# Kernel optimization log

Hardware: AMD Instinct MI355X
Metric: run time of the kernel (lower is better)

## Reference

```python
import jax, jax.numpy as jnp
import numpy as np
import math

B, N, D, H, HC = 2, 2048, 1024, 16, 8
HIDDEN = 4 * D
MAX_PERIOD = 10000.0


def _timestep_embedding(t, dim):
    half = dim // 2
    freqs = jnp.exp(-math.log(MAX_PERIOD) * jnp.arange(half, dtype=jnp.float32) / half)
    args = t[:, None] * freqs[None, :]
    return jnp.concatenate([jnp.cos(args), jnp.sin(args)], axis=-1)


def _layer_norm(x, scale, bias, eps=1e-6):
    mu = jnp.mean(x, axis=-1, keepdims=True)
    var = jnp.mean(jnp.square(x - mu), axis=-1, keepdims=True)
    return (x - mu) * jax.lax.rsqrt(var + eps) * scale + bias


def _modulate(x, shift, scale):
    return x * (1.0 + scale[:, None, :]) + shift[:, None, :]


def setup_inputs():
    key = jax.random.key(0)
    ks = jax.random.split(key, 16)

    def dense(k, fin, fout):
        return jax.random.normal(k, (fin, fout), dtype=jnp.float32) / np.sqrt(fin)

    return {
        'x': jax.random.normal(ks[0], (B, N, D), dtype=jnp.float32),
        't': jax.random.uniform(ks[1], (B,), dtype=jnp.float32) * 1000.0,
        'norm1_scale': jnp.ones((D,), jnp.float32),
        'norm1_bias': jnp.zeros((D,), jnp.float32),
        'norm2_scale': jnp.ones((D,), jnp.float32),
        'norm2_bias': jnp.zeros((D,), jnp.float32),
        'tc_w1': dense(ks[2], HIDDEN, HIDDEN),
        'tc_b1': jnp.zeros((HIDDEN,), jnp.float32),
        'tc_w2': dense(ks[3], HIDDEN, HIDDEN),
        'tc_b2': jnp.zeros((HIDDEN,), jnp.float32),
        'tc_wa': 0.02 * dense(ks[4], HIDDEN, 4 * D),
        'tc_ba': jnp.zeros((4 * D,), jnp.float32),
        'tc_wc': 0.02 * dense(ks[5], HIDDEN, 4 * D),
        'tc_bc': jnp.zeros((4 * D,), jnp.float32),
        'attn_qk_w': dense(ks[6], D, D),
        'attn_v_w': dense(ks[7], D, D),
        'attn_out_w': dense(ks[8], D, D),
        'doob_w': 0.02 * dense(ks[9], D, 1),
        'doob_b': jnp.zeros((1,), jnp.float32),
        'ch_qk_w': dense(ks[10], D, D),
        'ch_v_w': dense(ks[11], D, D),
        'ch_out_w': dense(ks[12], D, D),
        'tau': jnp.ones((HC, 1, 1), jnp.float32),
        'gamma1': 1e-4 * jnp.ones((D,), jnp.float32),
        'gamma2': 1e-4 * jnp.ones((D,), jnp.float32),
    }


def reference(x, t, norm1_scale, norm1_bias, norm2_scale, norm2_bias,
              tc_w1, tc_b1, tc_w2, tc_b2, tc_wa, tc_ba, tc_wc, tc_bc,
              attn_qk_w, attn_v_w, attn_out_w, doob_w, doob_b,
              ch_qk_w, ch_v_w, ch_out_w, tau, gamma1, gamma2):
    # ---- AdaLN time conditioning ----
    emb = _timestep_embedding(t, HIDDEN)                 # (B, HIDDEN)
    h = jax.nn.silu(emb @ tc_w1 + tc_b1)
    h = jax.nn.silu(h @ tc_w2 + tc_b2)
    a_shift, a_scale, a_gate, a_lg = jnp.split(h @ tc_wa + tc_ba, 4, axis=-1)
    c_shift, c_scale, c_gate, c_lg = jnp.split(h @ tc_wc + tc_bc, 4, axis=-1)

    # ---- token-diffusion attention (MHDM, tied Q=K, Doob tilt) ----
    x1 = _modulate(_layer_norm(x, norm1_scale, norm1_bias), a_shift, a_scale)
    qk = (x1 @ attn_qk_w) * jnp.exp(a_lg)[:, None, :]    # (B,N,D)
    v = x1 @ attn_v_w
    dh = D // H
    qh = qk.reshape(B, N, H, dh).transpose(0, 2, 1, 3)   # (B,H,N,dh)
    vh = v.reshape(B, N, H, dh).transpose(0, 2, 1, 3)
    dot = jnp.einsum('bhmd,bhnd->bhmn', qh, qh)
    q2 = jnp.sum(qh * qh, axis=-1)
    logits = 2.0 * dot - q2[:, :, :, None] - q2[:, :, None, :]
    phi = (x1 @ doob_w + doob_b)[..., 0]                 # (B,N) destination tilt
    logits = logits + phi[:, None, None, :]
    attn = jax.nn.softmax(logits, axis=-1)
    w = jnp.einsum('bhmn,bhnd->bhmd', attn, vh)
    attn_out = w.transpose(0, 2, 1, 3).reshape(B, N, D) @ attn_out_w
    x = x + attn_out * a_gate[:, None, :] * gamma1

    # ---- channel-diffusion attention ----
    x2 = _modulate(_layer_norm(x, norm2_scale, norm2_bias), c_shift, c_scale)
    qkc = (x2 @ ch_qk_w) * jnp.exp(c_lg)[:, None, :]
    vc = x2 @ ch_v_w
    dhc = D // HC
    qkc = qkc.transpose(0, 2, 1).reshape(B, HC, dhc, N)  # (B,HC,dhc,N)
    vc = vc.transpose(0, 2, 1).reshape(B, HC, dhc, N)
    dotc = jnp.einsum('bhcn,bhdn->bhcd', qkc, qkc)
    q2c = jnp.sum(qkc * qkc, axis=-1)                    # (B,HC,dhc)
    logitsc = (2.0 * dotc - q2c[:, :, :, None] - q2c[:, :, None, :]) / math.sqrt(N)
    logitsc = logitsc * tau[None, ...]
    attnc = jax.nn.softmax(logitsc, axis=-1)
    wc = jnp.einsum('bhcd,bhdn->bhcn', attnc, vc)
    ch_out = wc.reshape(B, D, N).transpose(0, 2, 1) @ ch_out_w
    x = x + ch_out * c_gate[:, None, :] * gamma2
    return x
```

## Files before the change

### kernel.cpp

```cpp
#include <hip/hip_runtime.h>
#include <hip/hip_bf16.h>
#include <math.h>

typedef __bf16 bf16;
typedef bf16 bf16x8 __attribute__((ext_vector_type(8)));
typedef bf16 bf16x2 __attribute__((ext_vector_type(2)));
typedef float f32x4 __attribute__((ext_vector_type(4)));

#define B_   2
#define N_   2048
#define D_   1024
#define H_   16
#define HC_  8
#define M_   (B_*N_)

__device__ __forceinline__ void gl16(const bf16* g, bf16* lds_base) {
#if __has_builtin(__builtin_amdgcn_global_load_lds)
  __builtin_amdgcn_global_load_lds((const __attribute__((address_space(1))) void*)g,
                                   (__attribute__((address_space(3))) void*)lds_base,
                                   16, 0, 0);
#else
  int lane = threadIdx.x & 63;
  *(uint4*)(lds_base + lane * 8) = *(const uint4*)g;
#endif
}

__device__ __forceinline__ bf16x2 cvt_pk_bf16(float lo, float hi) {
  unsigned int r;
  asm("v_cvt_pk_bf16_f32 %0, %1, %2" : "=v"(r) : "v"(lo), "v"(hi));
  union { unsigned int u; bf16x2 v; } c;
  c.u = r;
  return c.v;
}

__global__ __launch_bounds__(256) void emb_kernel(const float* __restrict__ tin,
                                                  float* __restrict__ emb) {
  int idx = blockIdx.x * 256 + threadIdx.x;
  int b = idx >> 12, p = idx & 4095;
  float tv = tin[b];
  int half = p & 2047;
  float freq = expf(-logf(10000.f) * (float)half * (1.f / 2048.f));
  float arg = tv * freq;
  emb[idx] = (p < 2048) ? cosf(arg) : sinf(arg);
}

__global__ __launch_bounds__(256) void gemv_kernel(const float* __restrict__ x,
                                                   const float* __restrict__ W,
                                                   float* __restrict__ part) {
  __shared__ float xs[2][64];
  int t = threadIdx.x;
  int j0 = blockIdx.x * 512;
  int k0 = blockIdx.y * 64;
  if (t < 64) xs[0][t] = x[k0 + t];
  else if (t < 128) xs[1][t - 64] = x[4096 + k0 + (t - 64)];
  __syncthreads();
  float a00 = 0.f, a01 = 0.f, a10 = 0.f, a11 = 0.f;
  int j = j0 + t * 2;
  #pragma unroll 8
  for (int k = 0; k < 64; k++) {
    float2 wv = *(const float2*)(W + (size_t)(k0 + k) * 4096 + j);
    float x0 = xs[0][k], x1 = xs[1][k];
    a00 += x0 * wv.x; a01 += x0 * wv.y;
    a10 += x1 * wv.x; a11 += x1 * wv.y;
  }
  *(float2*)(part + (size_t)(blockIdx.y * 2 + 0) * 4096 + j) = make_float2(a00, a01);
  *(float2*)(part + (size_t)(blockIdx.y * 2 + 1) * 4096 + j) = make_float2(a10, a11);
}

__global__ __launch_bounds__(256) void gemv_reduce_kernel(const float* __restrict__ part,
                                                          const float* __restrict__ bias,
                                                          float* __restrict__ y, int act) {
  int idx = blockIdx.x * 256 + threadIdx.x;
  int b = idx >> 12, j = idx & 4095;
  float s = bias[j];
  #pragma unroll
  for (int kc = 0; kc < 64; kc++) s += part[(size_t)(kc * 2 + b) * 4096 + j];
  if (act) s = s / (1.f + expf(-s));
  y[idx] = s;
}

__global__ __launch_bounds__(256) void postA_kernel(const float* __restrict__ avec,
                                                    const float* __restrict__ cvec,
                                                    const float* __restrict__ g1,
                                                    const float* __restrict__ g2,
                                                    float* __restrict__ sca, float* __restrict__ scc,
                                                    float* __restrict__ agv, float* __restrict__ cgv) {
  int idx = blockIdx.x * 256 + threadIdx.x;
  int b = idx >> 10, d = idx & 1023;
  sca[idx] = expf(avec[b * 4096 + 3072 + d]);
  scc[idx] = expf(cvec[b * 4096 + 3072 + d]);
  agv[idx] = avec[b * 4096 + 2048 + d] * g1[d];
  cgv[idx] = cvec[b * 4096 + 2048 + d] * g2[d];
}

__global__ __launch_bounds__(256) void wtconv6_kernel(const float* w0, const float* w1,
                                                      const float* w2, const float* w3,
                                                      const float* w4, const float* w5,
                                                      bf16* o0, bf16* o1, bf16* o2,
                                                      bf16* o3, bf16* o4, bf16* o5) {
  const float* W; bf16* Wt;
  switch (blockIdx.z) {
    case 0: W = w0; Wt = o0; break;
    case 1: W = w1; Wt = o1; break;
    case 2: W = w2; Wt = o2; break;
    case 3: W = w3; Wt = o3; break;
    case 4: W = w4; Wt = o4; break;
    default: W = w5; Wt = o5; break;
  }
  __shared__ float tile[32][33];
  int t = threadIdx.x;
  int i = t >> 5, j = t & 31;
  int n0 = blockIdx.x * 32, k0 = blockIdx.y * 32;
  #pragma unroll
  for (int u = 0; u < 4; u++) {
    int k = i + u * 8;
    tile[k][j] = W[(size_t)(k0 + k) * 1024 + n0 + j];
  }
  __syncthreads();
  #pragma unroll
  for (int u = 0; u < 4; u++) {
    int n = i + u * 8;
    Wt[(size_t)(n0 + n) * 1024 + k0 + j] = (bf16)tile[j][n];
  }
}

__global__ __launch_bounds__(256) void ln_mod_kernel(const float* __restrict__ xin,
                                                     const float* __restrict__ nsc,
                                                     const float* __restrict__ nbi,
                                                     const float* __restrict__ mod,
                                                     const float* __restrict__ doobw,
                                                     float* __restrict__ phi,
                                                     bf16* __restrict__ outp) {
  int row = blockIdx.x;
  int b = row >> 11;
  int t = threadIdx.x;
  const float* xr = xin + (size_t)row * 1024;
  float v[4], s = 0.f, ss = 0.f;
  #pragma unroll
  for (int u = 0; u < 4; u++) { v[u] = xr[t + u * 256]; s += v[u]; ss += v[u] * v[u]; }
  #pragma unroll
  for (int off = 1; off < 64; off <<= 1) { s += __shfl_xor(s, off, 64); ss += __shfl_xor(ss, off, 64); }
  __shared__ float sb[4], ssb[4], pb[4];
  if ((t & 63) == 0) { sb[t >> 6] = s; ssb[t >> 6] = ss; }
  __syncthreads();
  s = sb[0] + sb[1] + sb[2] + sb[3];
  ss = ssb[0] + ssb[1] + ssb[2] + ssb[3];
  float mu = s * (1.f / 1024.f);
  float var = ss * (1.f / 1024.f) - mu * mu;
  float rs = rsqrtf(var + 1e-6f);
  const float* shv = mod + b * 4096;
  const float* scv = mod + b * 4096 + 1024;
  float ph = 0.f;
  #pragma unroll
  for (int u = 0; u < 4; u++) {
    int d = t + u * 256;
    float y = (v[u] - mu) * rs * nsc[d] + nbi[d];
    float ym = y * (1.f + scv[d]) + shv[d];
    outp[(size_t)row * 1024 + d] = (bf16)ym;
    if (doobw) ph += ym * doobw[d];
  }
  if (doobw) {
    #pragma unroll
    for (int off = 1; off < 64; off <<= 1) ph += __shfl_xor(ph, off, 64);
    if ((t & 63) == 0) pb[t >> 6] = ph;
    __syncthreads();
    if (t == 0) phi[row] = pb[0] + pb[1] + pb[2] + pb[3];
  }
}

__global__ __launch_bounds__(256) void phimax_kernel(const float* __restrict__ phi,
                                                     float* __restrict__ pm) {
  int b = blockIdx.x;
  int t = threadIdx.x;
  float m = -1e30f;
  #pragma unroll
  for (int u = 0; u < 8; u++) m = fmaxf(m, phi[b * 2048 + t + u * 256]);
  #pragma unroll
  for (int off = 1; off < 64; off <<= 1) m = fmaxf(m, __shfl_xor(m, off, 64));
  __shared__ float mb[4];
  if ((t & 63) == 0) mb[t >> 6] = m;
  __syncthreads();
  if (t == 0) pm[b] = fmaxf(fmaxf(mb[0], mb[1]), fmaxf(mb[2], mb[3]));
}

template <int MODE, int TM>
__global__ __launch_bounds__(256) void gemm_kernel(const bf16* __restrict__ A,
                                                   const bf16* __restrict__ Wt,
                                                   const float* __restrict__ scale,
                                                   const float* __restrict__ resid,
                                                   void* __restrict__ out0,
                                                   void* __restrict__ out1) {
  constexpr int K = 1024;
  constexpr int WM = TM / 2;
  constexpr int IT = WM / 16;
  __shared__ bf16 As[TM * 64];
  __shared__ bf16 Bs[128 * 64];
  const int m0 = blockIdx.x * TM;
  const int n0 = blockIdx.y * 128;
  const int t = threadIdx.x, lane = t & 63, wid = t >> 6;
  const int wy = wid >> 1, wx = wid & 1;
  const int ml = lane & 15, quad = lane >> 4, rq = quad * 4, kq = quad * 8;
  const int srow = lane >> 3;
  const int schunk = (lane & 7) ^ srow;
  const bf16* gA = A  + (size_t)(m0 + wid * (TM / 4) + srow) * K + schunk * 8;
  const bf16* gB = Wt + (size_t)(n0 + wid * 32 + srow) * K + schunk * 8;
  bf16* lA = As + (wid * (TM / 4)) * 64;
  bf16* lB = Bs + (wid * 32) * 64;
  const int mlm = ml & 7;

  f32x4 acc[IT][4] = {};
  for (int k0 = 0; k0 < K; k0 += 64) {
    __syncthreads();
    #pragma unroll
    for (int q = 0; q < TM / 32; q++)
      gl16(gA + (size_t)q * 8 * K + k0, lA + q * 8 * 64);
    #pragma unroll
    for (int q = 0; q < 4; q++)
      gl16(gB + (size_t)q * 8 * K + k0, lB + q * 8 * 64);
    __syncthreads();
    #pragma unroll
    for (int ks = 0; ks < 2; ks++) {
      const int slot = ((ks * 4 + quad) ^ mlm) * 8;
      bf16x8 af[IT], bfv[4];
      #pragma unroll
      for (int i = 0; i < IT; i++)
        af[i] = *(const bf16x8*)(As + (wy * WM + i * 16 + ml) * 64 + slot);
      #pragma unroll
      for (int j = 0; j < 4; j++)
        bfv[j] = *(const bf16x8*)(Bs + (wx * 64 + j * 16 + ml) * 64 + slot);
      #pragma unroll
      for (int i = 0; i < IT; i++)
        #pragma unroll
        for (int j = 0; j < 4; j++)
          acc[i][j] = __builtin_amdgcn_mfma_f32_16x16x32_bf16(af[i], bfv[j], acc[i][j], 0, 0, 0);
    }
  }
  #pragma unroll
  for (int i = 0; i < IT; i++) {
    #pragma unroll
    for (int j = 0; j < 4; j++) {
      int col = n0 + wx * 64 + j * 16 + ml;
      #pragma unroll
      for (int r = 0; r < 4; r++) {
        int row = m0 + wy * WM + i * 16 + rq + r;
        int b = row >> 11, n = row & 2047;
        float val = acc[i][j][r];
        if constexpr (MODE == 10) {
          if (col < 1024) {
            ((bf16*)out0)[(size_t)row * 1024 + col] = (bf16)(val * scale[b * 1024 + col]);
          } else {
            int c2 = col - 1024;
            ((bf16*)out1)[((size_t)((b * 16 + (c2 >> 6)) * 64 + (c2 & 63))) * 2048 + n] = (bf16)val;
          }
        } else if constexpr (MODE == 11) {
          if (col < 1024) {
            float sv = val * scale[b * 1024 + col];
            ((bf16*)out0)[((size_t)((b * 8 + (col >> 7)) * 128 + (col & 127))) * 2048 + n] = (bf16)sv;
          } else {
            ((bf16*)out1)[(size_t)row * 1024 + (col - 1024)] = (bf16)val;
          }
        } else {
          float g = scale[b * 1024 + col];
          ((float*)out0)[(size_t)row * 1024 + col] =
              resid[(size_t)row * 1024 + col] + val * g;
        }
      }
    }
  }
}

__global__ __launch_bounds__(256) void q2e_kernel(const bf16* __restrict__ qk,
                                                  const float* __restrict__ phi,
                                                  const float* __restrict__ pm,
                                                  float* __restrict__ q2buf,
                                                  float* __restrict__ ebuf) {
  int row = blockIdx.x;
  int b = row >> 11, n = row & 2047;
  int t = threadIdx.x;
  const bf16* qr = qk + (size_t)row * 1024;
  __shared__ float q2s[16][17];
  {
    int h = t >> 4, i0 = (t & 15) * 4;
    float q = 0.f;
    #pragma unroll
    for (int u = 0; u < 4; u++) { float qv = (float)qr[h * 64 + i0 + u]; q += qv * qv; }
    q2s[h][t & 15] = q;
  }
  __syncthreads();
  if (t < 16) {
    float q2 = 0.f;
    #pragma unroll
    for (int u = 0; u < 16; u++) q2 += q2s[t][u];
    q2buf[(size_t)(b * 16 + t) * 2048 + n] = q2 * 1.44269504f;
    ebuf [(size_t)(b * 16 + t) * 2048 + n] = (phi[row] - q2 - pm[b]) * 1.44269504f;
  }
}

__global__ __launch_bounds__(512, 4) void flash_kernel(const bf16* __restrict__ qk,
                                                       const bf16* __restrict__ vt,
                                                       const float* __restrict__ q2buf,
                                                       const float* __restrict__ ebuf,
                                                       bf16* __restrict__ wout) {
  int mt = blockIdx.x, bh = blockIdx.y;
  int b = bh >> 4, h = bh & 15;
  int m0 = mt * 128;
  int t = threadIdx.x, lane = t & 63, w = t >> 6;
  int ml = lane & 15, quad = lane >> 4;
  int mlm = ml & 7, q1 = quad & 1, qh = quad >> 1;

  __shared__ __align__(16) bf16 Ks[2][64 * 64];
  __shared__ __align__(16) bf16 Vs[2][64 * 64];
  __shared__ __align__(16) bf16 Ps[8 * 16 * 64];

  int sr = lane >> 3, swz = (lane & 7) ^ sr;
  const bf16* gK = qk + (size_t)(b * 2048 + 8 * w + sr) * 1024 + h * 64 + swz * 8;
  const bf16* gV = vt + (size_t)(bh * 64 + 8 * w + sr) * 2048 + swz * 8;

  const bf16* qrow = qk + (size_t)(b * 2048 + m0 + w * 16 + ml) * 1024 + h * 64;
  bf16x8 qf0 = *(const bf16x8*)(qrow + quad * 8);
  bf16x8 qf1 = *(const bf16x8*)(qrow + 32 + quad * 8);

  float q2l = q2buf[(size_t)bh * 2048 + m0 + w * 16 + ml];
  const float* ep = ebuf + (size_t)bh * 2048;

  bf16* Pb = Ps + (w * 16 + ml) * 64;
  f32x4 oacc[4] = {};
  float rs = 0.f;

  gl16(gK, &Ks[0][w * 512]);
  gl16(gV, &Vs[0][w * 512]);

  #pragma unroll 2
  for (int nc = 0; nc < 32; nc++) {
    int cur = nc & 1;
    __syncthreads();
    if (nc + 1 < 32) {
      gl16(gK + (size_t)(nc + 1) * 64 * 1024, &Ks[cur ^ 1][w * 512]);
      gl16(gV + (nc + 1) * 64,                &Vs[cur ^ 1][w * 512]);
    }
    const bf16* Kc = Ks[cur];
    const bf16* Vc = Vs[cur];

    f32x4 sacc[4] = {};
    __builtin_amdgcn_s_setprio(1);
    #pragma unroll
    for (int ks = 0; ks < 2; ks++) {
      bf16x8 qb = ks ? qf1 : qf0;
      #pragma unroll
      for (int j = 0; j < 4; j++) {
        bf16x8 ka = *(const bf16x8*)(Kc + (j * 16 + ml) * 64 + ((4 * ks + quad) ^ mlm) * 8);
        sacc[j] = __builtin_amdgcn_mfma_f32_16x16x32_bf16(ka, qb, sacc[j], 0, 0, 0);
      }
    }
    __builtin_amdgcn_s_setprio(0);

    const float* epc = ep + nc * 64;
    #pragma unroll
    for (int j = 0; j < 4; j++) {
      float4 ev = *(const float4*)(epc + j * 16 + quad * 4);
      float p0 = exp2f(fmaf(2.88539008f, sacc[j][0], ev.x - q2l));
      float p1 = exp2f(fmaf(2.88539008f, sacc[j][1], ev.y - q2l));
      float p2 = exp2f(fmaf(2.88539008f, sacc[j][2], ev.z - q2l));
      float p3 = exp2f(fmaf(2.88539008f, sacc[j][3], ev.w - q2l));
      rs += (p0 + p1) + (p2 + p3);
      int sl = (((2 * j + qh) ^ mlm) * 4 + 2 * q1) * 2;
      *(bf16x2*)(Pb + sl)     = cvt_pk_bf16(p0, p1);
      *(bf16x2*)(Pb + sl + 2) = cvt_pk_bf16(p2, p3);
    }
    __builtin_amdgcn_sched_barrier(0);

    __builtin_amdgcn_s_setprio(1);
    #pragma unroll
    for (int ks = 0; ks < 2; ks++) {
      bf16x8 pa = *(const bf16x8*)(Pb + ((4 * ks + quad) ^ mlm) * 8);
      #pragma unroll
      for (int jd = 0; jd < 4; jd++) {
        bf16x8 vb = *(const bf16x8*)(Vc + (jd * 16 + ml) * 64 + ((4 * ks + quad) ^ mlm) * 8);
        oacc[jd] = __builtin_amdgcn_mfma_f32_16x16x32_bf16(pa, vb, oacc[jd], 0, 0, 0);
      }
    }
    __builtin_amdgcn_s_setprio(0);
  }

  rs += __shfl_xor(rs, 16, 64);
  rs += __shfl_xor(rs, 32, 64);
  float rinv = 1.f / rs;

  int rq = quad * 4;
  float rv[4];
  #pragma unroll
  for (int r = 0; r < 4; r++) rv[r] = __shfl(rinv, rq + r, 64);

  bf16* wrow = wout + (size_t)(b * 2048 + m0 + w * 16) * 1024 + h * 64;
  #pragma unroll
  for (int jd = 0; jd < 4; jd++)
    #pragma unroll
    for (int r = 0; r < 4; r++)
      wrow[(size_t)(rq + r) * 1024 + jd * 16 + ml] = (bf16)(oacc[jd][r] * rv[r]);
}

__global__ __launch_bounds__(256) void gram_kernel(const bf16* __restrict__ qkct,
                                                   float* __restrict__ dotp) {
  int bh = blockIdx.x, ksl = blockIdx.y;
  const bf16* Q = qkct + (size_t)bh * 128 * 2048 + ksl * 256;
  __shared__ bf16 Ts[128 * 40];
  int t = threadIdx.x, lane = t & 63, w = t >> 6;
  int ml = lane & 15, kq = (lane >> 4) * 8, rq = (lane >> 4) * 4;
  f32x4 acc[2][8] = {};
  for (int k0 = 0; k0 < 256; k0 += 32) {
    __syncthreads();
    #pragma unroll
    for (int u = 0; u < 2; u++) {
      int idx = u * 256 + t;
      int r = idx >> 2, seg = (idx & 3) * 8;
      *(uint4*)(Ts + r * 40 + seg) = *(const uint4*)(Q + (size_t)r * 2048 + k0 + seg);
    }
    __syncthreads();
    bf16x8 afr[2], bfr[8];
    #pragma unroll
    for (int i = 0; i < 2; i++) afr[i] = *(const bf16x8*)(Ts + (w * 32 + i * 16 + ml) * 40 + kq);
    #pragma unroll
    for (int j = 0; j < 8; j++) bfr[j] = *(const bf16x8*)(Ts + (j * 16 + ml) * 40 + kq);
    #pragma unroll
    for (int i = 0; i < 2; i++)
      #pragma unroll
      for (int j = 0; j < 8; j++)
        acc[i][j] = __builtin_amdgcn_mfma_f32_16x16x32_bf16(afr[i], bfr[j], acc[i][j], 0, 0, 0);
  }
  float* outp = dotp + ((size_t)ksl * 16 + bh) * 16384;
  #pragma unroll
  for (int i = 0; i < 2; i++)
    #pragma unroll
    for (int j = 0; j < 8; j++)
      #pragma unroll
      for (int r = 0; r < 4; r++) {
        int c = w * 32 + i * 16 + rq + r, d = j * 16 + ml;
        outp[c * 128 + d] = acc[i][j][r];
      }
}

__global__ __launch_bounds__(128) void chsm_kernel(const float* __restrict__ dotp,
                                                   const float* __restrict__ tau,
                                                   bf16* __restrict__ attnc) {
  int blk = blockIdx.x;
  int bh = blk >> 7, c = blk & 127, hc = bh & 7;
  int d = threadIdx.x;
  float dot = 0.f, dd = 0.f;
  #pragma unroll
  for (int kc = 0; kc < 8; kc++) {
    const float* pp = dotp + ((size_t)kc * 16 + bh) * 16384;
    dot += pp[c * 128 + d];
    dd  += pp[d * 128 + d];
  }
  __shared__ float diag[128];
  __shared__ float red[2], red2[2];
  diag[d] = dd;
  __syncthreads();
  float qc = diag[c];
  float sc = tau[hc] * rsqrtf(2048.f);
  float lg = sc * (2.f * dot - qc - dd);
  float mx = lg;
  #pragma unroll
  for (int off = 1; off < 64; off <<= 1) mx = fmaxf(mx, __shfl_xor(mx, off, 64));
  if ((d & 63) == 0) red[d >> 6] = mx;
  __syncthreads();
  mx = fmaxf(red[0], red[1]);
  float e = exp2f((lg - mx) * 1.44269504f);
  float sm = e;
  #pragma unroll
  for (int off = 1; off < 64; off <<= 1) sm += __shfl_xor(sm, off, 64);
  if ((d & 63) == 0) red2[d >> 6] = sm;
  __syncthreads();
  sm = red2[0] + red2[1];
  attnc[(size_t)bh * 16384 + c * 128 + d] = (bf16)(e / sm);
}

__global__ __launch_bounds__(256) void chav_kernel(const bf16* __restrict__ attnc,
                                                   const bf16* __restrict__ vc,
                                                   bf16* __restrict__ wcn) {
  int nb = blockIdx.x, bh = blockIdx.y;
  int b = bh >> 3, hc = bh & 7;
  int n0 = nb * 64;
  __shared__ bf16 As[128 * 136];
  __shared__ bf16 Bs[64 * 136];
  int t = threadIdx.x, lane = t & 63, w = t >> 6;
  int ml = lane & 15, kq = (lane >> 4) * 8, rq = (lane >> 4) * 4;
  #pragma unroll
  for (int u = 0; u < 8; u++) {
    int idx = u * 256 + t;
    int r = idx >> 4, seg = (idx & 15) * 8;
    *(uint4*)(As + r * 136 + seg) = *(const uint4*)(attnc + (size_t)bh * 16384 + r * 128 + seg);
  }
  #pragma unroll
  for (int u = 0; u < 4; u++) {
    int idx = u * 256 + t;
    int r = idx >> 4, seg = (idx & 15) * 8;
    *(uint4*)(Bs + r * 136 + seg) =
        *(const uint4*)(vc + (size_t)(b * 2048 + n0 + r) * 1024 + hc * 128 + seg);
  }
  __syncthreads();
  f32x4 acc[2][4] = {};
  #pragma unroll
  for (int ks = 0; ks < 4; ks++) {
    bf16x8 afr[2], bfr[4];
    #pragma unroll
    for (int i = 0; i < 2; i++)
      afr[i] = *(const bf16x8*)(As + (w * 32 + i * 16 + ml) * 136 + ks * 32 + kq);
    #pragma unroll
    for (int j = 0; j < 4; j++)
      bfr[j] = *(const bf16x8*)(Bs + (j * 16 + ml) * 136 + ks * 32 + kq);
    #pragma unroll
    for (int i = 0; i < 2; i++)
      #pragma unroll
      for (int j = 0; j < 4; j++)
        acc[i][j] = __builtin_amdgcn_mfma_f32_16x16x32_bf16(afr[i], bfr[j], acc[i][j], 0, 0, 0);
  }
  #pragma unroll
  for (int i = 0; i < 2; i++)
    #pragma unroll
    for (int j = 0; j < 4; j++)
      #pragma unroll
      for (int r = 0; r < 4; r++) {
        int c = w * 32 + i * 16 + rq + r;
        int n = n0 + j * 16 + ml;
        wcn[(size_t)(b * 2048 + n) * 1024 + hc * 128 + c] = (bf16)acc[i][j][r];
      }
}

extern "C" void kernel_launch(void* const* d_in, const int* in_sizes, int n_in,
                              void* d_out, int out_size, void* d_ws, size_t ws_size,
                              hipStream_t stream) {
  const float* x      = (const float*)d_in[0];
  const float* t      = (const float*)d_in[1];
  const float* n1s    = (const float*)d_in[2];
  const float* n1b    = (const float*)d_in[3];
  const float* n2s    = (const float*)d_in[4];
  const float* n2b    = (const float*)d_in[5];
  const float* tc_w1  = (const float*)d_in[6];
  const float* tc_b1  = (const float*)d_in[7];
  const float* tc_w2  = (const float*)d_in[8];
  const float* tc_b2  = (const float*)d_in[9];
  const float* tc_wa  = (const float*)d_in[10];
  const float* tc_ba  = (const float*)d_in[11];
  const float* tc_wc  = (const float*)d_in[12];
  const float* tc_bc  = (const float*)d_in[13];
  const float* aqk_w  = (const float*)d_in[14];
  const float* av_w   = (const float*)d_in[15];
  const float* aout_w = (const float*)d_in[16];
  const float* doobw  = (const float*)d_in[17];
  const float* cqk_w  = (const float*)d_in[19];
  const float* cv_w   = (const float*)d_in[20];
  const float* cout_w = (const float*)d_in[21];
  const float* tau    = (const float*)d_in[22];
  const float* g1     = (const float*)d_in[23];
  const float* g2     = (const float*)d_in[24];
  float* out = (float*)d_out;

  char* p = (char*)d_ws;
  auto alloc = [&](size_t bytes) -> void* {
    void* r = (void*)p;
    p += (bytes + 255) & ~(size_t)255;
    return r;
  };
  float* emb   = (float*)alloc(2 * 4096 * 4);
  float* h1    = (float*)alloc(2 * 4096 * 4);
  float* h2    = (float*)alloc(2 * 4096 * 4);
  float* avec  = (float*)alloc(2 * 4096 * 4);
  float* cvec  = (float*)alloc(2 * 4096 * 4);
  float* sca   = (float*)alloc(2 * 1024 * 4);
  float* scc   = (float*)alloc(2 * 1024 * 4);
  float* agv   = (float*)alloc(2 * 1024 * 4);
  float* cgv   = (float*)alloc(2 * 1024 * 4);
  float* phi   = (float*)alloc(4096 * 4);
  float* pmax  = (float*)alloc(2 * 4);
  float* q2buf = (float*)alloc(2 * 16 * 2048 * 4);
  float* ebuf  = (float*)alloc(2 * 16 * 2048 * 4);
  float* dotp  = (float*)alloc((size_t)8 * 16 * 16384 * 4);
  bf16* attnc  = (bf16*)alloc(16 * 128 * 128 * 2);
  bf16* wt     = (bf16*)alloc((size_t)6 * 1024 * 1024 * 2);
  bf16* xbf    = (bf16*)alloc((size_t)M_ * 1024 * 2);
  bf16* qkbf   = (bf16*)alloc((size_t)M_ * 1024 * 2);
  bf16* vbuf   = (bf16*)alloc((size_t)M_ * 1024 * 2);
  bf16* wbuf   = (bf16*)alloc((size_t)M_ * 1024 * 2);
  (void)ws_size; (void)in_sizes; (void)n_in; (void)out_size;

  float* partA = dotp;
  float* partB = dotp + (size_t)64 * 2 * 4096;

  bf16* wt_tok  = wt;
  bf16* wt_out  = wt + (size_t)2 * 1048576;
  bf16* wt_ch   = wt + (size_t)3 * 1048576;
  bf16* wt_cout = wt + (size_t)5 * 1048576;

  dim3 blk(256);
  wtconv6_kernel<<<dim3(32, 32, 6), blk, 0, stream>>>(
      aqk_w, av_w, aout_w, cqk_w, cv_w, cout_w,
      wt_tok, wt_tok + (size_t)1048576, wt_out,
      wt_ch,  wt_ch  + (size_t)1048576, wt_cout);

  emb_kernel<<<32, blk, 0, stream>>>(t, emb);
  gemv_kernel<<<dim3(8, 64), blk, 0, stream>>>(emb, tc_w1, partA);
  gemv_reduce_kernel<<<32, blk, 0, stream>>>(partA, tc_b1, h1, 1);
  gemv_kernel<<<dim3(8, 64), blk, 0, stream>>>(h1, tc_w2, partA);
  gemv_reduce_kernel<<<32, blk, 0, stream>>>(partA, tc_b2, h2, 1);
  gemv_kernel<<<dim3(8, 64), blk, 0, stream>>>(h2, tc_wa, partA);
  gemv_kernel<<<dim3(8, 64), blk, 0, stream>>>(h2, tc_wc, partB);
  gemv_reduce_kernel<<<32, blk, 0, stream>>>(partA, tc_ba, avec, 0);
  gemv_reduce_kernel<<<32, blk, 0, stream>>>(partB, tc_bc, cvec, 0);
  postA_kernel<<<8, blk, 0, stream>>>(avec, cvec, g1, g2, sca, scc, agv, cgv);

  ln_mod_kernel<<<4096, blk, 0, stream>>>(x, n1s, n1b, avec, doobw, phi, xbf);
  phimax_kernel<<<2, blk, 0, stream>>>(phi, pmax);
  gemm_kernel<10, 128><<<dim3(32, 16), blk, 0, stream>>>(xbf, wt_tok, sca, nullptr, qkbf, vbuf);
  q2e_kernel<<<4096, blk, 0, stream>>>(qkbf, phi, pmax, q2buf, ebuf);
  flash_kernel<<<dim3(16, 32), dim3(512), 0, stream>>>(qkbf, vbuf, q2buf, ebuf, wbuf);
  gemm_kernel<4, 64><<<dim3(64, 8), blk, 0, stream>>>(wbuf, wt_out, agv, x, out, nullptr);

  ln_mod_kernel<<<4096, blk, 0, stream>>>(out, n2s, n2b, cvec, nullptr, nullptr, xbf);
  gemm_kernel<11, 128><<<dim3(32, 16), blk, 0, stream>>>(xbf, wt_ch, scc, nullptr, qkbf, vbuf);
  gram_kernel<<<dim3(16, 8), blk, 0, stream>>>(qkbf, dotp);
  chsm_kernel<<<2048, dim3(128), 0, stream>>>(dotp, tau, attnc);
  chav_kernel<<<dim3(32, 16), blk, 0, stream>>>(attnc, vbuf, wbuf);
  gemm_kernel<4, 64><<<dim3(64, 8), blk, 0, stream>>>(wbuf, wt_cout, cgv, out, out, nullptr);
}
```

Measured before the change: 643.1 us.

## Store QK/V head-major and tiled for contiguous flash loads; halve GEMV split-K

The token QK projection is now written head-major as (b,h,n,64), and V is written in 64x64 tiles, so each flash-attention K/V chunk becomes one contiguous 8KB block instead of a strided gather. q2e is rewritten to read a contiguous 64-element row per thread and launches 16x fewer blocks. The timestep-MLP GEMVs use a K-split of 128 rather than 64, which halves the partial buffers and the reduction work. Those partial buffers get their own workspace allocation instead of aliasing dotp. The tradeoff is more scattered stores from the GEMM epilogue.

```diff
diff --git a/kernel.cpp b/kernel.cpp
--- a/kernel.cpp
+++ b/kernel.cpp
@@ -47,17 +47,17 @@
 __global__ __launch_bounds__(256) void gemv_kernel(const float* __restrict__ x,
                                                    const float* __restrict__ W,
                                                    float* __restrict__ part) {
-  __shared__ float xs[2][64];
+  __shared__ float xs[2][128];
   int t = threadIdx.x;
   int j0 = blockIdx.x * 512;
-  int k0 = blockIdx.y * 64;
-  if (t < 64) xs[0][t] = x[k0 + t];
-  else if (t < 128) xs[1][t - 64] = x[4096 + k0 + (t - 64)];
+  int k0 = blockIdx.y * 128;
+  if (t < 128) xs[0][t] = x[k0 + t];
+  else         xs[1][t - 128] = x[4096 + k0 + (t - 128)];
   __syncthreads();
   float a00 = 0.f, a01 = 0.f, a10 = 0.f, a11 = 0.f;
   int j = j0 + t * 2;
   #pragma unroll 8
-  for (int k = 0; k < 64; k++) {
+  for (int k = 0; k < 128; k++) {
     float2 wv = *(const float2*)(W + (size_t)(k0 + k) * 4096 + j);
     float x0 = xs[0][k], x1 = xs[1][k];
     a00 += x0 * wv.x; a01 += x0 * wv.y;
@@ -74,7 +74,7 @@
   int b = idx >> 12, j = idx & 4095;
   float s = bias[j];
   #pragma unroll
-  for (int kc = 0; kc < 64; kc++) s += part[(size_t)(kc * 2 + b) * 4096 + j];
+  for (int kc = 0; kc < 32; kc++) s += part[(size_t)(kc * 2 + b) * 4096 + j];
   if (act) s = s / (1.f + expf(-s));
   y[idx] = s;
 }
@@ -247,10 +247,14 @@
         float val = acc[i][j][r];
         if constexpr (MODE == 10) {
           if (col < 1024) {
-            ((bf16*)out0)[(size_t)row * 1024 + col] = (bf16)(val * scale[b * 1024 + col]);
+            int h = col >> 6, dh = col & 63;
+            ((bf16*)out0)[((size_t)(b * 16 + h) * 2048 + n) * 64 + dh] =
+                (bf16)(val * scale[b * 1024 + col]);
           } else {
             int c2 = col - 1024;
-            ((bf16*)out1)[((size_t)((b * 16 + (c2 >> 6)) * 64 + (c2 & 63))) * 2048 + n] = (bf16)val;
+            int h = c2 >> 6, dh = c2 & 63;
+            ((bf16*)out1)[(((size_t)(b * 16 + h) * 32 + (n >> 6)) * 64 + dh) * 64 + (n & 63)] =
+                (bf16)val;
           }
         } else if constexpr (MODE == 11) {
           if (col < 1024) {
@@ -269,35 +273,28 @@
   }
 }
 
-__global__ __launch_bounds__(256) void q2e_kernel(const bf16* __restrict__ qk,
+__global__ __launch_bounds__(256) void q2e_kernel(const bf16* __restrict__ qkh,
                                                   const float* __restrict__ phi,
                                                   const float* __restrict__ pm,
                                                   float* __restrict__ q2buf,
                                                   float* __restrict__ ebuf) {
-  int row = blockIdx.x;
-  int b = row >> 11, n = row & 2047;
-  int t = threadIdx.x;
-  const bf16* qr = qk + (size_t)row * 1024;
-  __shared__ float q2s[16][17];
-  {
-    int h = t >> 4, i0 = (t & 15) * 4;
-    float q = 0.f;
-    #pragma unroll
-    for (int u = 0; u < 4; u++) { float qv = (float)qr[h * 64 + i0 + u]; q += qv * qv; }
-    q2s[h][t & 15] = q;
-  }
-  __syncthreads();
-  if (t < 16) {
-    float q2 = 0.f;
-    #pragma unroll
-    for (int u = 0; u < 16; u++) q2 += q2s[t][u];
-    q2buf[(size_t)(b * 16 + t) * 2048 + n] = q2 * 1.44269504f;
-    ebuf [(size_t)(b * 16 + t) * 2048 + n] = (phi[row] - q2 - pm[b]) * 1.44269504f;
-  }
-}
-
-__global__ __launch_bounds__(512, 4) void flash_kernel(const bf16* __restrict__ qk,
-                                                       const bf16* __restrict__ vt,
+  int idx = blockIdx.x * 256 + threadIdx.x;
+  int bh = idx >> 11, n = idx & 2047;
+  int b = bh >> 4;
+  const bf16* qr = qkh + (size_t)idx * 64;
+  float q = 0.f;
+  #pragma unroll
+  for (int u = 0; u < 8; u++) {
+    bf16x8 v = *(const bf16x8*)(qr + u * 8);
+    #pragma unroll
+    for (int e = 0; e < 8; e++) { float f = (float)v[e]; q += f * f; }
+  }
+  q2buf[idx] = q * 1.44269504f;
+  ebuf[idx]  = (phi[b * 2048 + n] - q - pm[b]) * 1.44269504f;
+}
+
+__global__ __launch_bounds__(512, 4) void flash_kernel(const bf16* __restrict__ qkh,
+                                                       const bf16* __restrict__ vtb,
                                                        const float* __restrict__ q2buf,
                                                        const float* __restrict__ ebuf,
                                                        bf16* __restrict__ wout) {
@@ -313,10 +310,10 @@
   __shared__ __align__(16) bf16 Ps[8 * 16 * 64];
 
   int sr = lane >> 3, swz = (lane & 7) ^ sr;
-  const bf16* gK = qk + (size_t)(b * 2048 + 8 * w + sr) * 1024 + h * 64 + swz * 8;
-  const bf16* gV = vt + (size_t)(bh * 64 + 8 * w + sr) * 2048 + swz * 8;
-
-  const bf16* qrow = qk + (size_t)(b * 2048 + m0 + w * 16 + ml) * 1024 + h * 64;
+  const bf16* gK = qkh + ((size_t)bh * 2048 + 8 * w + sr) * 64 + swz * 8;
+  const bf16* gV = vtb + (size_t)bh * 32 * 4096 + (8 * w + sr) * 64 + swz * 8;
+
+  const bf16* qrow = qkh + ((size_t)bh * 2048 + m0 + w * 16 + ml) * 64;
   bf16x8 qf0 = *(const bf16x8*)(qrow + quad * 8);
   bf16x8 qf1 = *(const bf16x8*)(qrow + 32 + quad * 8);
 
@@ -335,8 +332,8 @@
     int cur = nc & 1;
     __syncthreads();
     if (nc + 1 < 32) {
-      gl16(gK + (size_t)(nc + 1) * 64 * 1024, &Ks[cur ^ 1][w * 512]);
-      gl16(gV + (nc + 1) * 64,                &Vs[cur ^ 1][w * 512]);
+      gl16(gK + (size_t)(nc + 1) * 4096, &Ks[cur ^ 1][w * 512]);
+      gl16(gV + (size_t)(nc + 1) * 4096, &Vs[cur ^ 1][w * 512]);
     }
     const bf16* Kc = Ks[cur];
     const bf16* Vc = Vs[cur];
@@ -563,6 +560,8 @@
     return r;
   };
   float* emb   = (float*)alloc(2 * 4096 * 4);
+  float* partA = (float*)alloc(32 * 2 * 4096 * 4);
+  float* partB = (float*)alloc(32 * 2 * 4096 * 4);
   float* h1    = (float*)alloc(2 * 4096 * 4);
   float* h2    = (float*)alloc(2 * 4096 * 4);
   float* avec  = (float*)alloc(2 * 4096 * 4);
@@ -584,9 +583,6 @@
   bf16* wbuf   = (bf16*)alloc((size_t)M_ * 1024 * 2);
   (void)ws_size; (void)in_sizes; (void)n_in; (void)out_size;
 
-  float* partA = dotp;
-  float* partB = dotp + (size_t)64 * 2 * 4096;
-
   bf16* wt_tok  = wt;
   bf16* wt_out  = wt + (size_t)2 * 1048576;
   bf16* wt_ch   = wt + (size_t)3 * 1048576;
@@ -599,12 +595,12 @@
       wt_ch,  wt_ch  + (size_t)1048576, wt_cout);
 
   emb_kernel<<<32, blk, 0, stream>>>(t, emb);
-  gemv_kernel<<<dim3(8, 64), blk, 0, stream>>>(emb, tc_w1, partA);
+  gemv_kernel<<<dim3(8, 32), blk, 0, stream>>>(emb, tc_w1, partA);
   gemv_reduce_kernel<<<32, blk, 0, stream>>>(partA, tc_b1, h1, 1);
-  gemv_kernel<<<dim3(8, 64), blk, 0, stream>>>(h1, tc_w2, partA);
+  gemv_kernel<<<dim3(8, 32), blk, 0, stream>>>(h1, tc_w2, partA);
   gemv_reduce_kernel<<<32, blk, 0, stream>>>(partA, tc_b2, h2, 1);
-  gemv_kernel<<<dim3(8, 64), blk, 0, stream>>>(h2, tc_wa, partA);
-  gemv_kernel<<<dim3(8, 64), blk, 0, stream>>>(h2, tc_wc, partB);
+  gemv_kernel<<<dim3(8, 32), blk, 0, stream>>>(h2, tc_wa, partA);
+  gemv_kernel<<<dim3(8, 32), blk, 0, stream>>>(h2, tc_wc, partB);
   gemv_reduce_kernel<<<32, blk, 0, stream>>>(partA, tc_ba, avec, 0);
   gemv_reduce_kernel<<<32, blk, 0, stream>>>(partB, tc_bc, cvec, 0);
   postA_kernel<<<8, blk, 0, stream>>>(avec, cvec, g1, g2, sca, scc, agv, cgv);
@@ -612,7 +608,7 @@
   ln_mod_kernel<<<4096, blk, 0, stream>>>(x, n1s, n1b, avec, doobw, phi, xbf);
   phimax_kernel<<<2, blk, 0, stream>>>(phi, pmax);
   gemm_kernel<10, 128><<<dim3(32, 16), blk, 0, stream>>>(xbf, wt_tok, sca, nullptr, qkbf, vbuf);
-  q2e_kernel<<<4096, blk, 0, stream>>>(qkbf, phi, pmax, q2buf, ebuf);
+  q2e_kernel<<<256, blk, 0, stream>>>(qkbf, phi, pmax, q2buf, ebuf);
   flash_kernel<<<dim3(16, 32), dim3(512), 0, stream>>>(qkbf, vbuf, q2buf, ebuf, wbuf);
   gemm_kernel<4, 64><<<dim3(64, 8), blk, 0, stream>>>(wbuf, wt_out, agv, x, out, nullptr);
 
```

After: 576.6 us. -10.3%, faster.
